# Performance work log

Hardware: AMD Instinct MI355X
Metric: run time of the kernel (lower is better)

## Reference

```python
import jax, jax.numpy as jnp
import numpy as np
from jax import lax

EPS = 1e-5
N_CROPS = 501
CROP_W = 500
RF = 65          # temporal receptive field
KS = 15          # conv1 kernel size
POOL = 3


def _bn(x, g, b, m, v, axis=1):
    shp = [1] * x.ndim
    shp[axis] = -1
    inv = g.reshape(shp) / jnp.sqrt(v.reshape(shp) + EPS)
    return (x - m.reshape(shp)) * inv + b.reshape(shp)


def setup_inputs() -> dict:
    key = jax.random.key(0)
    ks = jax.random.split(key, 16)
    B, C_IN, CH, T = 16, 1, 22, 1001
    F = 36
    OUT = 4
    FLAT = F * 43  # 1548 (corrected fc in_features; repo constant 504 is inconsistent)
    d = {
        "x": jax.random.normal(ks[0], (B, C_IN, CH, T), jnp.float32),
        # temporal conv [1,65]
        "w_t": jax.random.normal(ks[1], (F, 1, 1, RF), jnp.float32) * 0.1,
        "b_t": jax.random.normal(ks[2], (F,), jnp.float32) * 0.1,
        "bn_t_g": jax.random.uniform(ks[3], (F,), jnp.float32, 0.5, 1.5),
        "bn_t_b": jax.random.normal(ks[4], (F,), jnp.float32) * 0.1,
        "bn_t_m": jax.random.normal(ks[5], (F,), jnp.float32) * 0.1,
        "bn_t_v": jax.random.uniform(ks[6], (F,), jnp.float32, 0.5, 1.5),
        # spatial conv [22,1]
        "w_s": jax.random.normal(ks[7], (F, F, CH, 1), jnp.float32) * 0.05,
        "b_s": jax.random.normal(ks[8], (F,), jnp.float32) * 0.1,
        "bn_s_g": jax.random.uniform(ks[9], (F,), jnp.float32, 0.5, 1.5),
        "bn_s_b": jax.random.normal(ks[10], (F,), jnp.float32) * 0.1,
        "bn_s_m": jax.random.normal(ks[11], (F,), jnp.float32) * 0.1,
        "bn_s_v": jax.random.uniform(ks[12], (F,), jnp.float32, 0.5, 1.5),
        # conv1 [1,15] (as 1-D conv over time)
        "w_c": jax.random.normal(ks[13], (F, F, KS), jnp.float32) * 0.05,
        "b_c": jax.random.normal(ks[14], (F,), jnp.float32) * 0.1,
        "bn_c_g": jnp.ones((F,), jnp.float32),
        "bn_c_b": jnp.zeros((F,), jnp.float32),
        "bn_c_m": jnp.zeros((F,), jnp.float32),
        "bn_c_v": jnp.ones((F,), jnp.float32),
        # fc
        "w_fc": jax.random.normal(ks[15], (OUT, FLAT), jnp.float32) * 0.02,
        "b_fc": jnp.zeros((OUT,), jnp.float32),
    }
    return d


def reference(x, w_t, b_t, bn_t_g, bn_t_b, bn_t_m, bn_t_v,
              w_s, b_s, bn_s_g, bn_s_b, bn_s_m, bn_s_v,
              w_c, b_c, bn_c_g, bn_c_b, bn_c_m, bn_c_v,
              w_fc, b_fc):
    B = x.shape[0]
    F = w_t.shape[0]
    OUT = b_fc.shape[0]

    # temporal + spatial conv/BN/ELU are shift-invariant -> compute once over full T
    h = lax.conv_general_dilated(x, w_t, (1, 1), 'VALID',
                                 dimension_numbers=('NCHW', 'OIHW', 'NCHW'))
    h = h + b_t[None, :, None, None]                       # [B,36,22,937]
    h = jax.nn.elu(_bn(h, bn_t_g, bn_t_b, bn_t_m, bn_t_v))
    h = lax.conv_general_dilated(h, w_s, (1, 1), 'VALID',
                                 dimension_numbers=('NCHW', 'OIHW', 'NCHW'))
    h = h + b_s[None, :, None, None]                       # [B,36,1,937]
    h = jax.nn.elu(_bn(h, bn_s_g, bn_s_b, bn_s_m, bn_s_v))
    h = h[:, :, 0, :]                                      # [B,36,937]

    TW = CROP_W - RF + 1  # 436: temporal width of each crop after temporal conv

    def crop_logits(i):
        sl = lax.dynamic_slice_in_dim(h, i, TW, axis=2)    # [B,36,436]
        p1 = sl[:, :, :435].reshape(B, F, 145, POOL).mean(-1)  # avgpool1 -> [B,36,145]
        c = lax.conv_general_dilated(p1, w_c, (1,), 'VALID',
                                     dimension_numbers=('NCH', 'OIH', 'NCH'))
        c = c + b_c[None, :, None]                          # [B,36,131]
        c = jax.nn.elu(_bn(c, bn_c_g, bn_c_b, bn_c_m, bn_c_v))
        p2 = c[:, :, :129].reshape(B, F, 43, POOL).mean(-1)  # avgpool2 -> [B,36,43]
        flat = p2.reshape(B, -1)                            # [B,1548]
        return flat @ w_fc.T + b_fc                         # [B,OUT]

    def step(acc, i):
        return acc + crop_logits(i), None

    init = jnp.zeros((B, OUT), x.dtype)
    total, _ = lax.scan(step, init, jnp.arange(N_CROPS))
    return total / N_CROPS
```

## Files before the change

### kernel.cpp

```cpp
#include <hip/hip_runtime.h>

#define EPS 1e-5f
#define B 16
#define CH 22
#define CH2 24
#define T_IN 1001
#define F 36
#define RF 65
#define T1 937
#define FC 792
#define UN 885
#define PS3 112
#define KS 15
#define GN 295
#define WN 129
#define M43 43
#define BF 576
#define FLAT 1548

#define H2_OFF  0
#define A_OFF   539712
#define WTT_OFF 4617792
#define WST_OFF 4620132
#define WCT_OFF 4651236
#define BN_OFF  4670676

__device__ __forceinline__ float elu_f(float v) {
    return v > 0.f ? v : (__expf(v) - 1.f);
}

__global__ __launch_bounds__(256) void k_prep(
    const float* __restrict__ w_t, const float* __restrict__ w_s,
    const float* __restrict__ w_c,
    const float* __restrict__ b_t, const float* __restrict__ g_t,
    const float* __restrict__ be_t,const float* __restrict__ m_t,
    const float* __restrict__ v_t,
    const float* __restrict__ b_s, const float* __restrict__ g_s,
    const float* __restrict__ be_s,const float* __restrict__ m_s,
    const float* __restrict__ v_s,
    const float* __restrict__ b_c, const float* __restrict__ g_c,
    const float* __restrict__ be_c,const float* __restrict__ m_c,
    const float* __restrict__ v_c, const float* __restrict__ b_fc,
    float* __restrict__ wtT, float* __restrict__ wsTp,
    float* __restrict__ wcT, float* __restrict__ bnz,
    float* __restrict__ out)
{
    int i = blockIdx.x * 256 + threadIdx.x;
    if (i < F * RF)     { int k = i / F,  fi = i % F; wtT[i] = w_t[fi * RF + k]; }
    if (i < F * CH2 * F) {
        int fi = i / (CH2 * F);
        int r  = i % (CH2 * F);
        int ch = r / F, fo = r % F;
        wsTp[i] = (ch < CH) ? w_s[(fo * F + fi) * CH + ch] : 0.f;
    }
    if (i < F * KS * F) { int fk = i / F, fo = i % F; int f = fk / KS, k = fk % KS;
                          wcT[i] = w_c[(fo * F + f) * KS + k]; }
    if (i < F) {
        float s1 = g_t[i] * rsqrtf(v_t[i] + EPS);
        bnz[i]          = s1;
        bnz[F + i]      = (b_t[i] - m_t[i]) * s1 + be_t[i];
        float s2 = g_s[i] * rsqrtf(v_s[i] + EPS);
        bnz[2 * F + i]  = s2;
        bnz[3 * F + i]  = (b_s[i] - m_s[i]) * s2 + be_s[i];
        float s3 = g_c[i] * rsqrtf(v_c[i] + EPS);
        bnz[4 * F + i]  = s3;
        bnz[5 * F + i]  = (b_c[i] - m_c[i]) * s3 + be_c[i];
    }
    if (i < B * 4) out[i] = b_fc[i & 3];
}

__global__ __launch_bounds__(1024, 4) void k_fused(
    const float* __restrict__ x, const float* __restrict__ wtT,
    const float* __restrict__ wsTp, const float* __restrict__ bnz,
    float* __restrict__ h2)
{
    __shared__ float xs[CH2 * 128];
    __shared__ float comb[8][64][F];
    const int tid  = threadIdx.x;
    const int lane = tid & 63;
    const int w = __builtin_amdgcn_readfirstlane(tid >> 6);
    const int q = w >> 2;
    const int g = w & 3;
    const int b  = blockIdx.y;
    const int t0 = blockIdx.x * 64;

    for (int i = tid; i < CH2 * 128; i += 1024) {
        int ch = i >> 7, j = i & 127;
        int t = t0 + j; if (t > T_IN - 1) t = T_IN - 1;
        xs[i] = (ch < CH) ? x[(b * CH + ch) * T_IN + t] : 0.f;
    }
    __syncthreads();

    const int ch0 = q * 6;
    const int fi0 = g * 9;

    float acc[F];
    #pragma unroll
    for (int fo = 0; fo < F; ++fo) acc[fo] = 0.f;

    for (int c = 0; c < 6; ++c) {
        const float* xr = xs + (ch0 + c) * 128 + lane;

        float h1a[9];
        #pragma unroll
        for (int j = 0; j < 9; ++j) h1a[j] = 0.f;

        #pragma unroll 8
        for (int kp = 0; kp < 32; ++kp) {
            const int k = 2 * kp;
            float xv0 = xr[k];
            float xv1 = xr[k + 1];
            const float* w0 = wtT + k * F + fi0;
            const float* w1 = w0 + F;
            #pragma unroll
            for (int j = 0; j < 9; ++j) {
                h1a[j] += xv0 * w0[j];
                h1a[j] += xv1 * w1[j];
            }
        }
        {
            float xv = xr[64];
            const float* w64 = wtT + 64 * F + fi0;
            #pragma unroll
            for (int j = 0; j < 9; ++j) h1a[j] += xv * w64[j];
        }

        #pragma unroll
        for (int j = 0; j < 9; ++j)
            h1a[j] = elu_f(h1a[j] * bnz[fi0 + j] + bnz[F + fi0 + j]);

        #pragma unroll
        for (int j = 0; j < 9; ++j) {
            const float* wr = wsTp + ((fi0 + j) * CH2 + ch0 + c) * F;
            float e = h1a[j];
            #pragma unroll
            for (int fo = 0; fo < F; ++fo)
                acc[fo] += e * wr[fo];
        }
    }

    for (int half = 8; half >= 1; half >>= 1) {
        if (w >= half && w < 2 * half) {
            float4* cb = (float4*)&comb[w - half][lane][0];
            #pragma unroll
            for (int j = 0; j < 9; ++j)
                cb[j] = make_float4(acc[4*j], acc[4*j+1], acc[4*j+2], acc[4*j+3]);
        }
        __syncthreads();
        if (w < half) {
            const float4* cb = (const float4*)&comb[w][lane][0];
            #pragma unroll
            for (int j = 0; j < 9; ++j) {
                float4 v = cb[j];
                acc[4*j]   += v.x; acc[4*j+1] += v.y;
                acc[4*j+2] += v.z; acc[4*j+3] += v.w;
            }
        }
        __syncthreads();
    }

    if (w == 0) {
        int t = t0 + lane;
        if (t < T1) {
            #pragma unroll
            for (int fo = 0; fo < F; ++fo) {
                float s2 = bnz[2 * F + fo], o2 = bnz[3 * F + fo];
                h2[(b * F + fo) * T1 + t] = elu_f(acc[fo] * s2 + o2);
            }
        }
    }
}

__global__ __launch_bounds__(768, 3) void k_qconv(
    const float* __restrict__ h2, const float* __restrict__ wcT,
    const float* __restrict__ bnz, float* __restrict__ A)
{
    __shared__ float Ps[12][3][PS3];
    __shared__ float comb[6][64][F];
    const int tid  = threadIdx.x;
    const int lane = tid & 63;
    const int w = __builtin_amdgcn_readfirstlane(tid >> 6);
    const int b  = blockIdx.y;
    const int u0 = blockIdx.x * 64;
    const int f0 = w * 3;

    for (int i = lane; i < 3 * PS3; i += 64) {
        int fl = i / PS3, j = i % PS3;
        const float* hr = h2 + (size_t)(b * F + f0 + fl) * T1;
        int s = u0 + j;
        int s0 = s     < T1 - 1 ? s     : T1 - 1;
        int s1 = s + 1 < T1 - 1 ? s + 1 : T1 - 1;
        int s2 = s + 2 < T1 - 1 ? s + 2 : T1 - 1;
        Ps[w][fl][j] = (hr[s0] + hr[s1] + hr[s2]) * (1.f / 3.f);
    }

    float acc[F];
    #pragma unroll
    for (int j = 0; j < F; ++j) acc[j] = 0.f;

    #pragma unroll
    for (int fl = 0; fl < 3; ++fl) {
        #pragma unroll
        for (int k = 0; k < KS; ++k) {
            float pv = Ps[w][fl][lane + 3 * k];
            const float* wr = wcT + ((f0 + fl) * KS + k) * F;
            #pragma unroll
            for (int fo = 0; fo < F; ++fo) acc[fo] += pv * wr[fo];
        }
    }

    if (w >= 6) {
        float4* cb = (float4*)&comb[w - 6][lane][0];
        #pragma unroll
        for (int j = 0; j < 9; ++j)
            cb[j] = make_float4(acc[4*j], acc[4*j+1], acc[4*j+2], acc[4*j+3]);
    }
    __syncthreads();
    if (w < 6) {
        const float4* cb = (const float4*)&comb[w][lane][0];
        #pragma unroll
        for (int j = 0; j < 9; ++j) {
            float4 v = cb[j];
            acc[4*j] += v.x; acc[4*j+1] += v.y; acc[4*j+2] += v.z; acc[4*j+3] += v.w;
        }
    }
    __syncthreads();
    if (w >= 3 && w < 6) {
        float4* cb = (float4*)&comb[w - 3][lane][0];
        #pragma unroll
        for (int j = 0; j < 9; ++j)
            cb[j] = make_float4(acc[4*j], acc[4*j+1], acc[4*j+2], acc[4*j+3]);
    }
    __syncthreads();
    if (w < 3) {
        const float4* cb = (const float4*)&comb[w][lane][0];
        #pragma unroll
        for (int j = 0; j < 9; ++j) {
            float4 v = cb[j];
            acc[4*j] += v.x; acc[4*j+1] += v.y; acc[4*j+2] += v.z; acc[4*j+3] += v.w;
        }
    }
    __syncthreads();
    if (w == 1 || w == 2) {
        float4* cb = (float4*)&comb[w - 1][lane][0];
        #pragma unroll
        for (int j = 0; j < 9; ++j)
            cb[j] = make_float4(acc[4*j], acc[4*j+1], acc[4*j+2], acc[4*j+3]);
    }
    __syncthreads();
    if (w == 0) {
        #pragma unroll
        for (int j = 0; j < 9; ++j) {
            float4 v0 = ((const float4*)&comb[0][lane][0])[j];
            float4 v1 = ((const float4*)&comb[1][lane][0])[j];
            acc[4*j]   += v0.x + v1.x; acc[4*j+1] += v0.y + v1.y;
            acc[4*j+2] += v0.z + v1.z; acc[4*j+3] += v0.w + v1.w;
        }
        int u_g = u0 + lane;
        if (u_g < UN) {
            #pragma unroll
            for (int fo = 0; fo < F; ++fo) {
                float sc = bnz[4 * F + fo], oc = bnz[5 * F + fo];
                A[((size_t)(b * F + fo)) * UN + u_g] = elu_f(acc[fo] * sc + oc);
            }
        }
    }
}

__global__ __launch_bounds__(256) void k_wins(
    const float* __restrict__ A, const float* __restrict__ w_fc,
    float* __restrict__ out)
{
    __shared__ float Es[UN];
    __shared__ float G[GN];
    __shared__ float Ws[WN];
    __shared__ float Sm[M43];
    const int tid = threadIdx.x;
    const int bf = blockIdx.x;
    const int b = bf / F, f = bf % F;
    for (int i = tid; i < UN; i += 256)
        Es[i] = A[(size_t)bf * UN + i];
    __syncthreads();
    for (int q = tid; q < GN; q += 256)
        G[q] = Es[3 * q] + Es[3 * q + 1] + Es[3 * q + 2];
    __syncthreads();
    if (tid < WN) {
        float a = 0.f;
        for (int q = tid; q < tid + 167; ++q) a += G[q];
        Ws[tid] = a;
    }
    __syncthreads();
    if (tid < M43)
        Sm[tid] = (Ws[3 * tid] + Ws[3 * tid + 1] + Ws[3 * tid + 2]) * (1.f / 3.f);
    __syncthreads();
    if (tid < 4) {
        const float* wr = w_fc + tid * FLAT + f * M43;
        float a = 0.f;
        #pragma unroll 43
        for (int m = 0; m < M43; ++m) a += Sm[m] * wr[m];
        atomicAdd(&out[b * 4 + tid], a * (1.f / 501.f));
    }
}

extern "C" void kernel_launch(void* const* d_in, const int* in_sizes, int n_in,
                              void* d_out, int out_size, void* d_ws, size_t ws_size,
                              hipStream_t stream) {
    const float* x    = (const float*)d_in[0];
    const float* w_t  = (const float*)d_in[1];
    const float* b_t  = (const float*)d_in[2];
    const float* g_t  = (const float*)d_in[3];
    const float* be_t = (const float*)d_in[4];
    const float* m_t  = (const float*)d_in[5];
    const float* v_t  = (const float*)d_in[6];
    const float* w_s  = (const float*)d_in[7];
    const float* b_s  = (const float*)d_in[8];
    const float* g_s  = (const float*)d_in[9];
    const float* be_s = (const float*)d_in[10];
    const float* m_s  = (const float*)d_in[11];
    const float* v_s  = (const float*)d_in[12];
    const float* w_c  = (const float*)d_in[13];
    const float* b_c  = (const float*)d_in[14];
    const float* g_c  = (const float*)d_in[15];
    const float* be_c = (const float*)d_in[16];
    const float* m_c  = (const float*)d_in[17];
    const float* v_c  = (const float*)d_in[18];
    const float* w_fc = (const float*)d_in[19];
    const float* b_fc = (const float*)d_in[20];

    float* ws   = (float*)d_ws;
    float* h2   = ws + H2_OFF;
    float* A    = ws + A_OFF;
    float* wtT  = ws + WTT_OFF;
    float* wsTp = ws + WST_OFF;
    float* wcT  = ws + WCT_OFF;
    float* bnz  = ws + BN_OFF;
    float* out  = (float*)d_out;

    k_prep<<<dim3(128), 256, 0, stream>>>(
        w_t, w_s, w_c, b_t, g_t, be_t, m_t, v_t,
        b_s, g_s, be_s, m_s, v_s, b_c, g_c, be_c, m_c, v_c, b_fc,
        wtT, wsTp, wcT, bnz, out);

    k_fused<<<dim3(15, B), 1024, 0, stream>>>(x, wtT, wsTp, bnz, h2);
    k_qconv<<<dim3(14, B), 768, 0, stream>>>(h2, wcT, bnz, A);
    k_wins<<<dim3(BF), 256, 0, stream>>>(A, w_fc, out);
}
```

Before: 191.7 us.

## Load input directly to registers in fused conv and regroup temporal weights

The fused temporal+spatial conv kernel no longer stages the input tile in LDS. Each lane now reads its 65-sample window straight from global memory with float4 loads into registers. The temporal weights are re-laid out per filter group with pairs of taps interleaved and padded to 12, so weight reads can be wide uniform loads. The padded channels 22-23 are now skipped entirely. This removes the LDS fill, one barrier and the per-tap LDS reads, at the cost of redundant, unaligned global reads across lanes and higher register pressure from the 32-33 element x buffers.

```diff
diff --git a/kernel.cpp b/kernel.cpp
--- a/kernel.cpp
+++ b/kernel.cpp
@@ -20,10 +20,10 @@
 
 #define H2_OFF  0
 #define A_OFF   539712
-#define WTT_OFF 4617792
-#define WST_OFF 4620132
-#define WCT_OFF 4651236
-#define BN_OFF  4670676
+#define WTG_OFF 4617792
+#define WST_OFF 4620960
+#define WCT_OFF 4652064
+#define BN_OFF  4671504
 
 __device__ __forceinline__ float elu_f(float v) {
     return v > 0.f ? v : (__expf(v) - 1.f);
@@ -41,12 +41,19 @@
     const float* __restrict__ b_c, const float* __restrict__ g_c,
     const float* __restrict__ be_c,const float* __restrict__ m_c,
     const float* __restrict__ v_c, const float* __restrict__ b_fc,
-    float* __restrict__ wtT, float* __restrict__ wsTp,
+    float* __restrict__ wtG, float* __restrict__ wsTp,
     float* __restrict__ wcT, float* __restrict__ bnz,
     float* __restrict__ out)
 {
     int i = blockIdx.x * 256 + threadIdx.x;
-    if (i < F * RF)     { int k = i / F,  fi = i % F; wtT[i] = w_t[fi * RF + k]; }
+    if (i < 4 * 33 * 24) {
+        int g  = i / (33 * 24);
+        int r  = i % (33 * 24);
+        int kp = r / 24, slot = r % 24;
+        int kk = slot / 12, j = slot % 12;
+        int k  = 2 * kp + kk;
+        wtG[i] = (j < 9 && k < RF) ? w_t[(g * 9 + j) * RF + k] : 0.f;
+    }
     if (i < F * CH2 * F) {
         int fi = i / (CH2 * F);
         int r  = i % (CH2 * F);
@@ -70,11 +77,10 @@
 }
 
 __global__ __launch_bounds__(1024, 4) void k_fused(
-    const float* __restrict__ x, const float* __restrict__ wtT,
+    const float* __restrict__ x, const float* __restrict__ wtG,
     const float* __restrict__ wsTp, const float* __restrict__ bnz,
     float* __restrict__ h2)
 {
-    __shared__ float xs[CH2 * 128];
     __shared__ float comb[8][64][F];
     const int tid  = threadIdx.x;
     const int lane = tid & 63;
@@ -84,58 +90,75 @@
     const int b  = blockIdx.y;
     const int t0 = blockIdx.x * 64;
 
-    for (int i = tid; i < CH2 * 128; i += 1024) {
-        int ch = i >> 7, j = i & 127;
-        int t = t0 + j; if (t > T_IN - 1) t = T_IN - 1;
-        xs[i] = (ch < CH) ? x[(b * CH + ch) * T_IN + t] : 0.f;
-    }
-    __syncthreads();
+    int t  = t0 + lane;
+    int tcl = t < (T1 - 1) ? t : (T1 - 1);
 
     const int ch0 = q * 6;
     const int fi0 = g * 9;
+    const float* wgB = wtG + g * (33 * 24);
 
     float acc[F];
     #pragma unroll
     for (int fo = 0; fo < F; ++fo) acc[fo] = 0.f;
 
     for (int c = 0; c < 6; ++c) {
-        const float* xr = xs + (ch0 + c) * 128 + lane;
-
-        float h1a[9];
-        #pragma unroll
-        for (int j = 0; j < 9; ++j) h1a[j] = 0.f;
-
-        #pragma unroll 8
-        for (int kp = 0; kp < 32; ++kp) {
-            const int k = 2 * kp;
-            float xv0 = xr[k];
-            float xv1 = xr[k + 1];
-            const float* w0 = wtT + k * F + fi0;
-            const float* w1 = w0 + F;
+        const int ch = ch0 + c;
+        if (ch < CH) {
+            const float* xp = x + (b * CH + ch) * T_IN + tcl;
+
+            float h1a[9];
+            #pragma unroll
+            for (int j = 0; j < 9; ++j) h1a[j] = 0.f;
+
+            {
+                float xv[32];
+                #pragma unroll
+                for (int m = 0; m < 8; ++m) {
+                    float4 v = *(const float4*)(xp + 4 * m);
+                    xv[4*m] = v.x; xv[4*m+1] = v.y; xv[4*m+2] = v.z; xv[4*m+3] = v.w;
+                }
+                #pragma unroll
+                for (int kp = 0; kp < 16; ++kp) {
+                    const float* wp = wgB + kp * 24;
+                    float x0 = xv[2*kp], x1 = xv[2*kp+1];
+                    #pragma unroll
+                    for (int j = 0; j < 9; ++j)
+                        h1a[j] += x0 * wp[j] + x1 * wp[12 + j];
+                }
+            }
+            {
+                float xv[33];
+                #pragma unroll
+                for (int m = 0; m < 8; ++m) {
+                    float4 v = *(const float4*)(xp + 32 + 4 * m);
+                    xv[4*m] = v.x; xv[4*m+1] = v.y; xv[4*m+2] = v.z; xv[4*m+3] = v.w;
+                }
+                xv[32] = xp[64];
+                #pragma unroll
+                for (int kp = 0; kp < 16; ++kp) {
+                    const float* wp = wgB + (16 + kp) * 24;
+                    float x0 = xv[2*kp], x1 = xv[2*kp+1];
+                    #pragma unroll
+                    for (int j = 0; j < 9; ++j)
+                        h1a[j] += x0 * wp[j] + x1 * wp[12 + j];
+                }
+                const float* wp = wgB + 32 * 24;
+                #pragma unroll
+                for (int j = 0; j < 9; ++j) h1a[j] += xv[32] * wp[j];
+            }
+
+            #pragma unroll
+            for (int j = 0; j < 9; ++j)
+                h1a[j] = elu_f(h1a[j] * bnz[fi0 + j] + bnz[F + fi0 + j]);
+
             #pragma unroll
             for (int j = 0; j < 9; ++j) {
-                h1a[j] += xv0 * w0[j];
-                h1a[j] += xv1 * w1[j];
-            }
-        }
-        {
-            float xv = xr[64];
-            const float* w64 = wtT + 64 * F + fi0;
-            #pragma unroll
-            for (int j = 0; j < 9; ++j) h1a[j] += xv * w64[j];
-        }
-
-        #pragma unroll
-        for (int j = 0; j < 9; ++j)
-            h1a[j] = elu_f(h1a[j] * bnz[fi0 + j] + bnz[F + fi0 + j]);
-
-        #pragma unroll
-        for (int j = 0; j < 9; ++j) {
-            const float* wr = wsTp + ((fi0 + j) * CH2 + ch0 + c) * F;
-            float e = h1a[j];
-            #pragma unroll
-            for (int fo = 0; fo < F; ++fo)
-                acc[fo] += e * wr[fo];
+                const float* wr = wsTp + ((fi0 + j) * CH2 + ch) * F;
+                float e = h1a[j];
+                #pragma unroll
+                for (int fo = 0; fo < F; ++fo)
+                    acc[fo] += e * wr[fo];
+            }
         }
     }
 
@@ -160,7 +183,6 @@
     }
 
     if (w == 0) {
-        int t = t0 + lane;
         if (t < T1) {
             #pragma unroll
             for (int fo = 0; fo < F; ++fo) {
@@ -330,7 +352,7 @@
     float* ws   = (float*)d_ws;
     float* h2   = ws + H2_OFF;
     float* A    = ws + A_OFF;
-    float* wtT  = ws + WTT_OFF;
+    float* wtG  = ws + WTG_OFF;
     float* wsTp = ws + WST_OFF;
     float* wcT  = ws + WCT_OFF;
     float* bnz  = ws + BN_OFF;
@@ -339,9 +361,9 @@
     k_prep<<<dim3(128), 256, 0, stream>>>(
         w_t, w_s, w_c, b_t, g_t, be_t, m_t, v_t,
         b_s, g_s, be_s, m_s, v_s, b_c, g_c, be_c, m_c, v_c, b_fc,
-        wtT, wsTp, wcT, bnz, out);
-
-    k_fused<<<dim3(15, B), 1024, 0, stream>>>(x, wtT, wsTp, bnz, h2);
+        wtG, wsTp, wcT, bnz, out);
+
+    k_fused<<<dim3(15, B), 1024, 0, stream>>>(x, wtG, wsTp, bnz, h2);
     k_qconv<<<dim3(14, B), 768, 0, stream>>>(h2, wcT, bnz, A);
     k_wins<<<dim3(BF), 256, 0, stream>>>(A, w_fc, out);
 }
```

Result: slower. 249.0 us (+29.9%).

## Split qconv by output channel and precompute pooled rows in a separate kernel

Applied to the files above, without the earlier changes.

Moves the 3-tap average pooling of h2 into a new k_pool kernel that writes a padded pooled buffer P to global memory. k_qconv is restructured so each wavefront owns three output channels and loops over all 36 input channels. This removes the per-block shared-memory staging and the multi-step LDS reduction tree across wavefronts. Weights are repacked into a padded [12][36][15][4] layout. The cost is an extra kernel launch, an extra global round trip for P, and a reduction loop that now reads global memory directly.

```diff
diff --git a/kernel.cpp b/kernel.cpp
--- a/kernel.cpp
+++ b/kernel.cpp
@@ -10,7 +10,7 @@
 #define T1 937
 #define FC 792
 #define UN 885
-#define PS3 112
+#define PSP 944
 #define KS 15
 #define GN 295
 #define WN 129
@@ -20,10 +20,11 @@
 
 #define H2_OFF  0
 #define A_OFF   539712
+#define P_OFF   1049472
 #define WTT_OFF 4617792
 #define WST_OFF 4620132
-#define WCT_OFF 4651236
-#define BN_OFF  4670676
+#define WCQ_OFF 4651236
+#define BN_OFF  4677156
 
 __device__ __forceinline__ float elu_f(float v) {
     return v > 0.f ? v : (__expf(v) - 1.f);
@@ -42,7 +43,7 @@
     const float* __restrict__ be_c,const float* __restrict__ m_c,
     const float* __restrict__ v_c, const float* __restrict__ b_fc,
     float* __restrict__ wtT, float* __restrict__ wsTp,
-    float* __restrict__ wcT, float* __restrict__ bnz,
+    float* __restrict__ wcQ, float* __restrict__ bnz,
     float* __restrict__ out)
 {
     int i = blockIdx.x * 256 + threadIdx.x;
@@ -53,8 +54,14 @@
         int ch = r / F, fo = r % F;
         wsTp[i] = (ch < CH) ? w_s[(fo * F + fi) * CH + ch] : 0.f;
     }
-    if (i < F * KS * F) { int fk = i / F, fo = i % F; int f = fk / KS, k = fk % KS;
-                          wcT[i] = w_c[(fo * F + f) * KS + k]; }
+    if (i < 12 * 36 * 15 * 4) {
+        int t3 = i / (36 * 15 * 4);
+        int r  = i % (36 * 15 * 4);
+        int f  = r / 60;
+        int r2 = r % 60;
+        int k  = r2 / 4, j = r2 % 4;
+        wcQ[i] = (j < 3) ? w_c[((3 * t3 + j) * F + f) * KS + k] : 0.f;
+    }
     if (i < F) {
         float s1 = g_t[i] * rsqrtf(v_t[i] + EPS);
         bnz[i]          = s1;
@@ -171,99 +178,55 @@
     }
 }
 
-__global__ __launch_bounds__(768, 3) void k_qconv(
-    const float* __restrict__ h2, const float* __restrict__ wcT,
+__global__ __launch_bounds__(256) void k_pool(
+    const float* __restrict__ h2, float* __restrict__ P)
+{
+    const int bf = blockIdx.x;
+    const float* hr = h2 + (size_t)bf * T1;
+    float* Pr = P + (size_t)bf * PSP;
+    for (int i = threadIdx.x; i < PSP; i += 256) {
+        int s0 = i     < T1 - 1 ? i     : T1 - 1;
+        int s1 = i + 1 < T1 - 1 ? i + 1 : T1 - 1;
+        int s2 = i + 2 < T1 - 1 ? i + 2 : T1 - 1;
+        Pr[i] = (hr[s0] + hr[s1] + hr[s2]) * (1.f / 3.f);
+    }
+}
+
+__global__ __launch_bounds__(768) void k_qconv(
+    const float* __restrict__ P, const float* __restrict__ wcQ,
     const float* __restrict__ bnz, float* __restrict__ A)
 {
-    __shared__ float Ps[12][3][PS3];
-    __shared__ float comb[6][64][F];
     const int tid  = threadIdx.x;
     const int lane = tid & 63;
-    const int w = __builtin_amdgcn_readfirstlane(tid >> 6);
+    const int t3 = __builtin_amdgcn_readfirstlane(tid >> 6);
     const int b  = blockIdx.y;
     const int u0 = blockIdx.x * 64;
-    const int f0 = w * 3;
-
-    for (int i = lane; i < 3 * PS3; i += 64) {
-        int fl = i / PS3, j = i % PS3;
-        const float* hr = h2 + (size_t)(b * F + f0 + fl) * T1;
-        int s = u0 + j;
-        int s0 = s     < T1 - 1 ? s     : T1 - 1;
-        int s1 = s + 1 < T1 - 1 ? s + 1 : T1 - 1;
-        int s2 = s + 2 < T1 - 1 ? s + 2 : T1 - 1;
-        Ps[w][fl][j] = (hr[s0] + hr[s1] + hr[s2]) * (1.f / 3.f);
-    }
-
-    float acc[F];
-    #pragma unroll
-    for (int j = 0; j < F; ++j) acc[j] = 0.f;
-
-    #pragma unroll
-    for (int fl = 0; fl < 3; ++fl) {
+    const int fo0 = t3 * 3;
+
+    const float* wq = wcQ + t3 * (36 * 60);
+
+    float a0 = 0.f, a1 = 0.f, a2 = 0.f;
+
+    for (int f = 0; f < F; ++f) {
+        const float* Pr = P + (size_t)(b * F + f) * PSP + u0 + lane;
+        const float* wf = wq + f * 60;
         #pragma unroll
         for (int k = 0; k < KS; ++k) {
-            float pv = Ps[w][fl][lane + 3 * k];
-            const float* wr = wcT + ((f0 + fl) * KS + k) * F;
-            #pragma unroll
-            for (int fo = 0; fo < F; ++fo) acc[fo] += pv * wr[fo];
-        }
-    }
-
-    if (w >= 6) {
-        float4* cb = (float4*)&comb[w - 6][lane][0];
-        #pragma unroll
-        for (int j = 0; j < 9; ++j)
-            cb[j] = make_float4(acc[4*j], acc[4*j+1], acc[4*j+2], acc[4*j+3]);
-    }
-    __syncthreads();
-    if (w < 6) {
-        const float4* cb = (const float4*)&comb[w][lane][0];
-        #pragma unroll
-        for (int j = 0; j < 9; ++j) {
-            float4 v = cb[j];
-            acc[4*j] += v.x; acc[4*j+1] += v.y; acc[4*j+2] += v.z; acc[4*j+3] += v.w;
-        }
-    }
-    __syncthreads();
-    if (w >= 3 && w < 6) {
-        float4* cb = (float4*)&comb[w - 3][lane][0];
-        #pragma unroll
-        for (int j = 0; j < 9; ++j)
-            cb[j] = make_float4(acc[4*j], acc[4*j+1], acc[4*j+2], acc[4*j+3]);
-    }
-    __syncthreads();
-    if (w < 3) {
-        const float4* cb = (const float4*)&comb[w][lane][0];
-        #pragma unroll
-        for (int j = 0; j < 9; ++j) {
-            float4 v = cb[j];
-            acc[4*j] += v.x; acc[4*j+1] += v.y; acc[4*j+2] += v.z; acc[4*j+3] += v.w;
-        }
-    }
-    __syncthreads();
-    if (w == 1 || w == 2) {
-        float4* cb = (float4*)&comb[w - 1][lane][0];
-        #pragma unroll
-        for (int j = 0; j < 9; ++j)
-            cb[j] = make_float4(acc[4*j], acc[4*j+1], acc[4*j+2], acc[4*j+3]);
-    }
-    __syncthreads();
-    if (w == 0) {
-        #pragma unroll
-        for (int j = 0; j < 9; ++j) {
-            float4 v0 = ((const float4*)&comb[0][lane][0])[j];
-            float4 v1 = ((const float4*)&comb[1][lane][0])[j];
-            acc[4*j]   += v0.x + v1.x; acc[4*j+1] += v0.y + v1.y;
-            acc[4*j+2] += v0.z + v1.z; acc[4*j+3] += v0.w + v1.w;
-        }
-        int u_g = u0 + lane;
-        if (u_g < UN) {
-            #pragma unroll
-            for (int fo = 0; fo < F; ++fo) {
-                float sc = bnz[4 * F + fo], oc = bnz[5 * F + fo];
-                A[((size_t)(b * F + fo)) * UN + u_g] = elu_f(acc[fo] * sc + oc);
-            }
-        }
+            float pv = Pr[3 * k];
+            a0 += pv * wf[4 * k + 0];
+            a1 += pv * wf[4 * k + 1];
+            a2 += pv * wf[4 * k + 2];
+        }
+    }
+
+    int u = u0 + lane;
+    if (u < UN) {
+        float sc0 = bnz[4 * F + fo0 + 0], oc0 = bnz[5 * F + fo0 + 0];
+        float sc1 = bnz[4 * F + fo0 + 1], oc1 = bnz[5 * F + fo0 + 1];
+        float sc2 = bnz[4 * F + fo0 + 2], oc2 = bnz[5 * F + fo0 + 2];
+        A[((size_t)(b * F + fo0 + 0)) * UN + u] = elu_f(a0 * sc0 + oc0);
+        A[((size_t)(b * F + fo0 + 1)) * UN + u] = elu_f(a1 * sc1 + oc1);
+        A[((size_t)(b * F + fo0 + 2)) * UN + u] = elu_f(a2 * sc2 + oc2);
     }
 }
 
@@ -330,18 +293,20 @@
     float* ws   = (float*)d_ws;
     float* h2   = ws + H2_OFF;
     float* A    = ws + A_OFF;
+    float* P    = ws + P_OFF;
     float* wtT  = ws + WTT_OFF;
     float* wsTp = ws + WST_OFF;
-    float* wcT  = ws + WCT_OFF;
+    float* wcQ  = ws + WCQ_OFF;
     float* bnz  = ws + BN_OFF;
     float* out  = (float*)d_out;
 
     k_prep<<<dim3(128), 256, 0, stream>>>(
         w_t, w_s, w_c, b_t, g_t, be_t, m_t, v_t,
         b_s, g_s, be_s, m_s, v_s, b_c, g_c, be_c, m_c, v_c, b_fc,
-        wtT, wsTp, wcT, bnz, out);
+        wtT, wsTp, wcQ, bnz, out);
 
     k_fused<<<dim3(15, B), 1024, 0, stream>>>(x, wtT, wsTp, bnz, h2);
-    k_qconv<<<dim3(14, B), 768, 0, stream>>>(h2, wcT, bnz, A);
+    k_pool<<<dim3(BF), 256, 0, stream>>>(h2, P);
+    k_qconv<<<dim3(14, B), 768, 0, stream>>>(P, wcQ, bnz, A);
     k_wins<<<dim3(BF), 256, 0, stream>>>(A, w_fc, out);
 }
```

Measured after the change: 200.3 us. +4.5%, slower.
